# Performance work log

Hardware: AMD Instinct MI355X
Metric: run time of the kernel (lower is better)

The kernel has to match this reference:

```python
import jax, jax.numpy as jnp
import numpy as np

N = 100000       # nodes
E0 = 1600000     # random edges (self-loops appended -> E = E0 + N)
IN = 128         # input feature dim
H1, C1 = 8, 8    # conv1 heads, out channels per head
C2 = 64          # num_classes (conv2 out, heads=1)
NEG_SLOPE = 0.2


def gat_conv(x, src, dst, W, att_src, att_dst, bias, heads, out_ch, concat):
    """PyG-style GATConv (eval mode, no dropout). x: [N, F_in]."""
    n = x.shape[0]
    h = (x @ W).reshape(n, heads, out_ch)              # [N, H, C]
    a_src = jnp.sum(h * att_src, axis=-1)              # [N, H]
    a_dst = jnp.sum(h * att_dst, axis=-1)              # [N, H]
    e = jax.nn.leaky_relu(a_src[src] + a_dst[dst], NEG_SLOPE)  # [E, H]
    # segment softmax over edges grouped by destination node
    e_max = jax.ops.segment_max(e, dst, num_segments=n)
    ex = jnp.exp(e - e_max[dst])
    denom = jax.ops.segment_sum(ex, dst, num_segments=n)
    alpha = ex / denom[dst]                            # [E, H]
    msg = h[src] * alpha[:, :, None]                   # [E, H, C]
    out = jax.ops.segment_sum(msg, dst, num_segments=n)  # [N, H, C]
    out = out.reshape(n, heads * out_ch) if concat else out.mean(axis=1)
    return out + bias


def setup_inputs() -> dict:
    key = jax.random.key(0)
    ks = jax.random.split(key, 12)
    nodes = jnp.arange(N, dtype=jnp.int32)
    feat = jax.random.normal(ks[0], (N, IN), jnp.float32)
    src = jax.random.randint(ks[1], (E0,), 0, N, jnp.int32)
    dst = jax.random.randint(ks[2], (E0,), 0, N, jnp.int32)
    loop = jnp.arange(N, dtype=jnp.int32)
    edge_index = jnp.stack([jnp.concatenate([src, loop]),
                            jnp.concatenate([dst, loop])])  # [2, E]
    mask = jnp.ones((N,), bool)
    label = jax.random.randint(ks[3], (N,), 0, C2, jnp.int32)
    s = 0.1
    W1 = jax.random.normal(ks[4], (IN, H1 * C1), jnp.float32) * s
    att_src1 = jax.random.normal(ks[5], (H1, C1), jnp.float32) * s
    att_dst1 = jax.random.normal(ks[6], (H1, C1), jnp.float32) * s
    b1 = jnp.zeros((H1 * C1,), jnp.float32)
    W2 = jax.random.normal(ks[7], (H1 * C1, C2), jnp.float32) * s
    att_src2 = jax.random.normal(ks[8], (1, C2), jnp.float32) * s
    att_dst2 = jax.random.normal(ks[9], (1, C2), jnp.float32) * s
    b2 = jnp.zeros((C2,), jnp.float32)
    return {"nodes": nodes, "feat": feat, "edge_index": edge_index, "mask": mask,
            "label": label, "W1": W1, "att_src1": att_src1, "att_dst1": att_dst1,
            "b1": b1, "W2": W2, "att_src2": att_src2, "att_dst2": att_dst2, "b2": b2}


def reference(nodes, feat, edge_index, mask, label,
              W1, att_src1, att_dst1, b1, W2, att_src2, att_dst2, b2):
    src, dst = edge_index[0], edge_index[1]
    x = jax.nn.elu(gat_conv(feat, src, dst, W1, att_src1, att_dst1, b1,
                            H1, C1, concat=True))          # [N, 64]
    scores = gat_conv(x, src, dst, W2, att_src2, att_dst2, b2,
                      1, C2, concat=False)                  # [N, C2]
    logp = jax.nn.log_softmax(scores, axis=-1)
    nll = -jnp.take_along_axis(logp, label[:, None].astype(jnp.int32), axis=1)[:, 0]
    m = mask.astype(scores.dtype)
    loss = jnp.sum(nll * m) / jnp.sum(m)                    # masked mean CE
    pred = jnp.argmax(scores, axis=1)
    return loss, pred, label
```

## Files before the change

kernel.cpp:

```cpp
#include <hip/hip_runtime.h>
#include <cstdint>

#define NHEAD 8
#define D1 64
#define IN_F 128
#define NEG 0.2f
#define NBINS 256
#define BINS 1024
#define BSH 7
#define CHUNK 8192

__device__ __forceinline__ void fma4(float4& a, float s, const float4& v)
{
    a.x = fmaf(s, v.x, a.x); a.y = fmaf(s, v.y, a.y);
    a.z = fmaf(s, v.z, a.z); a.w = fmaf(s, v.w, a.w);
}

__global__ __launch_bounds__(256) void k_gemm1_hist(
    const float* __restrict__ feat,
    const float* __restrict__ W1,
    const float* __restrict__ att_s,
    const float* __restrict__ att_d,
    float* __restrict__ h1, float* __restrict__ a_src, float* __restrict__ a_dst,
    const int* __restrict__ dst, int* __restrict__ btot, int* __restrict__ bh,
    int N, int E, int GH)
{
    __shared__ float Wh[32 * 64];
    __shared__ float Fh[64 * 36];
    const int tid = threadIdx.x;

    if ((int)blockIdx.x < GH) {
        int* hist = (int*)Wh;
        for (int b = tid; b < BINS; b += 256) hist[b] = 0;
        __syncthreads();
        const int e0 = blockIdx.x * CHUNK;
        #pragma unroll
        for (int r = 0; r < 8; ++r) {
            int e = e0 + r * 1024 + tid * 4;
            if (e + 3 < E) {
                int4 d4 = *(const int4*)&dst[e];
                atomicAdd(&hist[d4.x >> BSH], 1);
                atomicAdd(&hist[d4.y >> BSH], 1);
                atomicAdd(&hist[d4.z >> BSH], 1);
                atomicAdd(&hist[d4.w >> BSH], 1);
            } else {
                for (int k = e; k < E && k < e + 4; ++k)
                    atomicAdd(&hist[dst[k] >> BSH], 1);
            }
        }
        __syncthreads();
        for (int b = tid; b < BINS; b += 256) {
            int c = hist[b];
            bh[(size_t)blockIdx.x * BINS + b] = c;
            if (c) atomicAdd(&btot[b * 16], c);
        }
        return;
    }

    const int tx = tid & 15, ty = tid >> 4;
    const int base = (blockIdx.x - GH) * 64;
    float4 acc0 = {0,0,0,0}, acc1 = {0,0,0,0}, acc2 = {0,0,0,0}, acc3 = {0,0,0,0};

    for (int p = 0; p < 4; ++p) {
        if (p) __syncthreads();
        for (int i = tid; i < 32 * 64; i += 256)
            Wh[i] = W1[p * 2048 + i];
        for (int i = tid; i < 64 * 32; i += 256) {
            int r = i >> 5, kk = i & 31;
            int n = base + r;
            Fh[r * 36 + kk] = (n < N) ? feat[(size_t)n * IN_F + p * 32 + kk] : 0.f;
        }
        __syncthreads();
        const float* wk = &Wh[4 * tx];
        const float* f0 = &Fh[(4 * ty + 0) * 36];
        const float* f1 = &Fh[(4 * ty + 1) * 36];
        const float* f2 = &Fh[(4 * ty + 2) * 36];
        const float* f3 = &Fh[(4 * ty + 3) * 36];
        #pragma unroll
        for (int kk = 0; kk < 32; kk += 4) {
            float4 fa = *(const float4*)&f0[kk];
            float4 fb = *(const float4*)&f1[kk];
            float4 fc = *(const float4*)&f2[kk];
            float4 fd = *(const float4*)&f3[kk];
            float4 w0 = *(const float4*)&wk[(kk + 0) * 64];
            float4 w1 = *(const float4*)&wk[(kk + 1) * 64];
            float4 w2 = *(const float4*)&wk[(kk + 2) * 64];
            float4 w3 = *(const float4*)&wk[(kk + 3) * 64];
            fma4(acc0, fa.x, w0); fma4(acc0, fa.y, w1); fma4(acc0, fa.z, w2); fma4(acc0, fa.w, w3);
            fma4(acc1, fb.x, w0); fma4(acc1, fb.y, w1); fma4(acc1, fb.z, w2); fma4(acc1, fb.w, w3);
            fma4(acc2, fc.x, w0); fma4(acc2, fc.y, w1); fma4(acc2, fc.z, w2); fma4(acc2, fc.w, w3);
            fma4(acc3, fd.x, w0); fma4(acc3, fd.y, w1); fma4(acc3, fd.z, w2); fma4(acc3, fd.w, w3);
        }
    }
    const float4 as4 = *(const float4*)&att_s[4 * tx];
    const float4 ad4 = *(const float4*)&att_d[4 * tx];
    float4 accs[4] = {acc0, acc1, acc2, acc3};
    #pragma unroll
    for (int i = 0; i < 4; ++i) {
        int n = base + 4 * ty + i;
        if (n < N) {
            *(float4*)&h1[(size_t)n * D1 + 4 * tx] = accs[i];
            float ps = accs[i].x * as4.x + accs[i].y * as4.y + accs[i].z * as4.z + accs[i].w * as4.w;
            float pd = accs[i].x * ad4.x + accs[i].y * ad4.y + accs[i].z * ad4.z + accs[i].w * ad4.w;
            ps += __shfl_xor(ps, 1);
            pd += __shfl_xor(pd, 1);
            if ((tx & 1) == 0) {
                a_src[n * NHEAD + (tx >> 1)] = ps;
                a_dst[n * NHEAD + (tx >> 1)] = pd;
            }
        }
    }
}

__device__ __forceinline__ int block_incl_scan(int v, int tid, int* lds4)
{
    int lane = tid & 63, w = tid >> 6;
    #pragma unroll
    for (int off = 1; off < 64; off <<= 1) {
        int t = __shfl_up(v, off);
        if (lane >= off) v += t;
    }
    if (lane == 63) lds4[w] = v;
    __syncthreads();
    int add = 0;
    #pragma unroll
    for (int i = 0; i < 4; ++i)
        if (i < w) add += lds4[i];
    __syncthreads();
    return v + add;
}

__global__ __launch_bounds__(256) void k_bscan(
    const int* __restrict__ btot, int* __restrict__ bbase, int* __restrict__ gcur,
    double* __restrict__ bins)
{
    __shared__ int lds4[4];
    const int tid = threadIdx.x;
    bins[tid] = 0.0;
    int c0 = btot[(4 * tid + 0) * 16];
    int c1 = btot[(4 * tid + 1) * 16];
    int c2 = btot[(4 * tid + 2) * 16];
    int c3 = btot[(4 * tid + 3) * 16];
    int v = c0 + c1 + c2 + c3;
    int incl = block_incl_scan(v, tid, lds4);
    int b0 = incl - v, b1 = b0 + c0, b2 = b1 + c1, b3 = b2 + c2;
    bbase[4 * tid + 0] = b0; gcur[(4 * tid + 0) * 16] = b0;
    bbase[4 * tid + 1] = b1; gcur[(4 * tid + 1) * 16] = b1;
    bbase[4 * tid + 2] = b2; gcur[(4 * tid + 2) * 16] = b2;
    bbase[4 * tid + 3] = b3; gcur[(4 * tid + 3) * 16] = b3;
}

__global__ __launch_bounds__(256) void k_scatter(
    const int* __restrict__ src, const int* __restrict__ dst,
    const int* __restrict__ bh, int* __restrict__ gcur,
    int* __restrict__ bucketed, int E)
{
    __shared__ int base[BINS], cur[BINS];
    const int tid = threadIdx.x;
    for (int b = tid; b < BINS; b += 256) {
        cur[b] = 0;
        int c = bh[(size_t)blockIdx.x * BINS + b];
        if (c) base[b] = atomicAdd(&gcur[b * 16], c);
    }
    __syncthreads();
    const int e0 = blockIdx.x * CHUNK;
    #pragma unroll
    for (int r = 0; r < 8; ++r) {
        int e = e0 + r * 1024 + tid * 4;
        if (e + 3 < E) {
            int4 d4 = *(const int4*)&dst[e];
            int4 s4 = *(const int4*)&src[e];
            int bx, rx;
            bx = d4.x >> BSH; rx = atomicAdd(&cur[bx], 1); bucketed[base[bx] + rx] = ((d4.x & 127) << 17) | s4.x;
            bx = d4.y >> BSH; rx = atomicAdd(&cur[bx], 1); bucketed[base[bx] + rx] = ((d4.y & 127) << 17) | s4.y;
            bx = d4.z >> BSH; rx = atomicAdd(&cur[bx], 1); bucketed[base[bx] + rx] = ((d4.z & 127) << 17) | s4.z;
            bx = d4.w >> BSH; rx = atomicAdd(&cur[bx], 1); bucketed[base[bx] + rx] = ((d4.w & 127) << 17) | s4.w;
        } else {
            for (int k = e; k < E && k < e + 4; ++k) {
                int d = dst[k];
                int bx = d >> BSH;
                int rx = atomicAdd(&cur[bx], 1);
                bucketed[base[bx] + rx] = ((d & 127) << 17) | src[k];
            }
        }
    }
}

__global__ __launch_bounds__(256) void k_seg(
    const int* __restrict__ btot, const int* __restrict__ bbase,
    const int* __restrict__ bucketed,
    int* __restrict__ deg, int* __restrict__ rowstart, int* __restrict__ srcs, int N)
{
    __shared__ int cnt[128], cur[128], lb[128];
    const int tid = threadIdx.x;
    const int b = blockIdx.x;
    const int gs = bbase[b];
    const int sz = btot[b * 16];
    if (tid < 128) { cnt[tid] = 0; cur[tid] = 0; }
    __syncthreads();
    for (int i = tid; i < sz; i += 256)
        atomicAdd(&cnt[bucketed[gs + i] >> 17], 1);
    __syncthreads();
    if (tid < 128) lb[tid] = cnt[tid];
    __syncthreads();
    #pragma unroll
    for (int off = 1; off < 128; off <<= 1) {
        int t = 0;
        if (tid < 128 && tid >= off) t = lb[tid - off];
        __syncthreads();
        if (tid < 128 && tid >= off) lb[tid] += t;
        __syncthreads();
    }
    if (tid < 128) {
        int ex = lb[tid] - cnt[tid];
        lb[tid] = ex;
        int d = b * 128 + tid;
        if (d < N) { deg[d] = cnt[tid]; rowstart[d] = gs + ex; }
    }
    __syncthreads();
    for (int i = tid; i < sz; i += 256) {
        int v = bucketed[gs + i];
        int d7 = v >> 17;
        int r = atomicAdd(&cur[d7], 1);
        srcs[gs + lb[d7] + r] = v & 0x1FFFF;
    }
}

__global__ __launch_bounds__(256) void k_agg1(
    const int* __restrict__ deg, const int* __restrict__ rowstart,
    const int* __restrict__ srcs,
    const float* __restrict__ a_s, const float* __restrict__ a_d,
    const float* __restrict__ h1, const float* __restrict__ b1,
    float* __restrict__ x, int N)
{
    const int tid = threadIdx.x, w = tid >> 6, j = tid & 63;
    const int c = j & 7, hh = j >> 3;
    const int n = blockIdx.x * 4 + w;
    if (n >= N) return;
    const int rlen = deg[n];
    const int row = rowstart[n];
    const float ad = a_d[n * NHEAD + hh];
    float acc0 = 0.f, acc1 = 0.f, den = 0.f;
    int m = rlen < 8 ? rlen : 8;
    int myS   = (c < m) ? srcs[row + c] : 0;
    float av  = (c < m) ? a_s[myS * NHEAD + hh] : 0.f;
    for (int base = 0; base < rlen; base += 8) {
        int mn = rlen - base - 8; if (mn > 8) mn = 8;
        int   myS_n = (c < mn) ? srcs[row + base + 8 + c] : 0;
        float av_n  = (c < mn) ? a_s[myS_n * NHEAD + hh] : 0.f;
        float ex = 0.f;
        if (c < m) {
            float v = av + ad;
            v = v > 0.f ? v : NEG * v;
            ex = expf(v);
        }
        float ds = ex;
        ds += __shfl_xor(ds, 1);
        ds += __shfl_xor(ds, 2);
        ds += __shfl_xor(ds, 4);
        den += ds;
        if (m == 8) {
            int   s8[8]; float e8[8], l8[8];
            #pragma unroll
            for (int k = 0; k < 8; ++k) {
                s8[k] = __builtin_amdgcn_readlane(myS, k);
                e8[k] = __shfl(ex, (j & 0x38) | k);
            }
            #pragma unroll
            for (int k = 0; k < 8; ++k)
                l8[k] = h1[(size_t)s8[k] * D1 + j];
            #pragma unroll
            for (int k = 0; k < 8; ++k) {
                if (k & 1) acc1 = fmaf(e8[k], l8[k], acc1);
                else       acc0 = fmaf(e8[k], l8[k], acc0);
            }
        } else {
            for (int k = 0; k < m; ++k) {
                int s = __shfl(myS, k);
                float exk = __shfl(ex, (j & 0x38) | k);
                if (k & 1) acc1 = fmaf(exk, h1[(size_t)s * D1 + j], acc1);
                else       acc0 = fmaf(exk, h1[(size_t)s * D1 + j], acc0);
            }
        }
        myS = myS_n; av = av_n; m = mn > 0 ? mn : 0;
    }
    float o = (acc0 + acc1) / den + b1[j];
    x[(size_t)n * D1 + j] = o > 0.f ? o : expm1f(o);
}

__global__ __launch_bounds__(256) void k_gemm2(
    const float* __restrict__ x,
    const float* __restrict__ W2,
    const float* __restrict__ att_s,
    const float* __restrict__ att_d,
    float* __restrict__ h2, float* __restrict__ a_src, float* __restrict__ a_dst,
    int N)
{
    __shared__ float Wh[64 * 64];
    __shared__ float Fh[64 * 68];
    const int tid = threadIdx.x;
    const int tx = tid & 15, ty = tid >> 4;
    const int base = blockIdx.x * 64;
    for (int i = tid; i < 64 * 64; i += 256)
        Wh[i] = W2[i];
    for (int i = tid; i < 64 * 64; i += 256) {
        int r = i >> 6, kk = i & 63;
        int n = base + r;
        Fh[r * 68 + kk] = (n < N) ? x[(size_t)n * 64 + kk] : 0.f;
    }
    __syncthreads();
    float4 acc0 = {0,0,0,0}, acc1 = {0,0,0,0}, acc2 = {0,0,0,0}, acc3 = {0,0,0,0};
    const float* wk = &Wh[4 * tx];
    const float* f0 = &Fh[(4 * ty + 0) * 68];
    const float* f1 = &Fh[(4 * ty + 1) * 68];
    const float* f2 = &Fh[(4 * ty + 2) * 68];
    const float* f3 = &Fh[(4 * ty + 3) * 68];
    #pragma unroll 4
    for (int kk = 0; kk < 64; kk += 4) {
        float4 fa = *(const float4*)&f0[kk];
        float4 fb = *(const float4*)&f1[kk];
        float4 fc = *(const float4*)&f2[kk];
        float4 fd = *(const float4*)&f3[kk];
        float4 w0 = *(const float4*)&wk[(kk + 0) * 64];
        float4 w1 = *(const float4*)&wk[(kk + 1) * 64];
        float4 w2 = *(const float4*)&wk[(kk + 2) * 64];
        float4 w3 = *(const float4*)&wk[(kk + 3) * 64];
        fma4(acc0, fa.x, w0); fma4(acc0, fa.y, w1); fma4(acc0, fa.z, w2); fma4(acc0, fa.w, w3);
        fma4(acc1, fb.x, w0); fma4(acc1, fb.y, w1); fma4(acc1, fb.z, w2); fma4(acc1, fb.w, w3);
        fma4(acc2, fc.x, w0); fma4(acc2, fc.y, w1); fma4(acc2, fc.z, w2); fma4(acc2, fc.w, w3);
        fma4(acc3, fd.x, w0); fma4(acc3, fd.y, w1); fma4(acc3, fd.z, w2); fma4(acc3, fd.w, w3);
    }
    const float4 as4 = *(const float4*)&att_s[4 * tx];
    const float4 ad4 = *(const float4*)&att_d[4 * tx];
    float4 accs[4] = {acc0, acc1, acc2, acc3};
    #pragma unroll
    for (int i = 0; i < 4; ++i) {
        int n = base + 4 * ty + i;
        if (n < N) {
            *(float4*)&h2[(size_t)n * 64 + 4 * tx] = accs[i];
            float ps = accs[i].x * as4.x + accs[i].y * as4.y + accs[i].z * as4.z + accs[i].w * as4.w;
            float pd = accs[i].x * ad4.x + accs[i].y * ad4.y + accs[i].z * ad4.z + accs[i].w * ad4.w;
            ps += __shfl_xor(ps, 1); pd += __shfl_xor(pd, 1);
            ps += __shfl_xor(ps, 2); pd += __shfl_xor(pd, 2);
            ps += __shfl_xor(ps, 4); pd += __shfl_xor(pd, 4);
            ps += __shfl_xor(ps, 8); pd += __shfl_xor(pd, 8);
            if (tx == 0) { a_src[n] = ps; a_dst[n] = pd; }
        }
    }
}

__global__ __launch_bounds__(256) void k_agg2(
    const int* __restrict__ deg, const int* __restrict__ rowstart,
    const int* __restrict__ srcs,
    const float* __restrict__ a_s, const float* __restrict__ a_d,
    const float* __restrict__ h2, const float* __restrict__ b2,
    const int* __restrict__ label,
    float* __restrict__ dout, double* __restrict__ bins, int N)
{
    __shared__ float snll[4];
    const int tid = threadIdx.x, w = tid >> 6, j = tid & 63;
    const int t = j & 15, q = j >> 4;
    const int n = blockIdx.x * 4 + w;
    if (j == 0) snll[w] = 0.f;
    if (n < N) {
        const int rlen = deg[n];
        const int row = rowstart[n];
        const float ad = a_d[n];
        float4 acc = {0.f, 0.f, 0.f, 0.f};
        float den = 0.f;
        for (int base = 0; base < rlen; base += 64) {
            int m = rlen - base; if (m > 64) m = 64;
            int myS = 0; float ex = 0.f;
            if (j < m) {
                myS = srcs[row + base + j];
                float v = a_s[myS] + ad;
                v = v > 0.f ? v : NEG * v;
                ex = expf(v);
            }
            float ds = ex;
            #pragma unroll
            for (int off = 1; off < 64; off <<= 1) ds += __shfl_xor(ds, off);
            den += ds;
            int eb = 0;
            for (; eb + 16 <= m; eb += 16) {
                int s4[4]; float e4[4]; float4 l4[4];
                #pragma unroll
                for (int ii = 0; ii < 4; ++ii) {
                    int e = eb + 4 * ii + q;
                    s4[ii] = __shfl(myS, e);
                    e4[ii] = __shfl(ex, e);
                }
                #pragma unroll
                for (int ii = 0; ii < 4; ++ii)
                    l4[ii] = *(const float4*)&h2[(size_t)s4[ii] * 64 + 4 * t];
                #pragma unroll
                for (int ii = 0; ii < 4; ++ii)
                    fma4(acc, e4[ii], l4[ii]);
            }
            for (; eb + 4 <= m; eb += 4) {
                int e = eb + q;
                int sk = __shfl(myS, e);
                float ek = __shfl(ex, e);
                float4 lk = *(const float4*)&h2[(size_t)sk * 64 + 4 * t];
                fma4(acc, ek, lk);
            }
            for (int k = eb; k < m; ++k) {
                int sk = __shfl(myS, k);
                float ek = __shfl(ex, k);
                if (q == (k & 3)) {
                    float4 lk = *(const float4*)&h2[(size_t)sk * 64 + 4 * t];
                    fma4(acc, ek, lk);
                }
            }
        }
        acc.x += __shfl_xor(acc.x, 16); acc.y += __shfl_xor(acc.y, 16);
        acc.z += __shfl_xor(acc.z, 16); acc.w += __shfl_xor(acc.w, 16);
        acc.x += __shfl_xor(acc.x, 32); acc.y += __shfl_xor(acc.y, 32);
        acc.z += __shfl_xor(acc.z, 32); acc.w += __shfl_xor(acc.w, 32);
        float4 b = *(const float4*)&b2[4 * t];
        float4 sc;
        sc.x = acc.x / den + b.x; sc.y = acc.y / den + b.y;
        sc.z = acc.z / den + b.z; sc.w = acc.w / den + b.w;
        float mv = sc.x; int mi = 4 * t;
        if (sc.y > mv) { mv = sc.y; mi = 4 * t + 1; }
        if (sc.z > mv) { mv = sc.z; mi = 4 * t + 2; }
        if (sc.w > mv) { mv = sc.w; mi = 4 * t + 3; }
        #pragma unroll
        for (int off = 1; off < 16; off <<= 1) {
            float ov = __shfl_xor(mv, off);
            int oi = __shfl_xor(mi, off);
            if (ov > mv || (ov == mv && oi < mi)) { mv = ov; mi = oi; }
        }
        float se = expf(sc.x - mv) + expf(sc.y - mv) + expf(sc.z - mv) + expf(sc.w - mv);
        #pragma unroll
        for (int off = 1; off < 16; off <<= 1) se += __shfl_xor(se, off);
        int lab = label[n];
        int comp = lab & 3;
        float cl = comp == 0 ? sc.x : comp == 1 ? sc.y : comp == 2 ? sc.z : sc.w;
        float sl = __shfl(cl, (j & 0x30) | (lab >> 2));
        if (j == 0) {
            snll[w] = mv + logf(se) - sl;
            dout[1 + n] = (float)mi;
            dout[1 + (size_t)N + n] = (float)lab;
        }
    }
    __syncthreads();
    if (tid == 0) {
        double bsum4 = (double)snll[0] + (double)snll[1]
                     + (double)snll[2] + (double)snll[3];
        atomicAdd(&bins[blockIdx.x & (NBINS - 1)], bsum4);
    }
}

__global__ __launch_bounds__(256) void k_loss(
    const double* __restrict__ bins, float* __restrict__ dout, int N)
{
    __shared__ double sw[4];
    const int tid = threadIdx.x;
    double v = bins[tid];
    #pragma unroll
    for (int off = 1; off < 64; off <<= 1) v += __shfl_xor(v, off);
    if ((tid & 63) == 0) sw[tid >> 6] = v;
    __syncthreads();
    if (tid == 0)
        dout[0] = (float)((sw[0] + sw[1] + sw[2] + sw[3]) / (double)N);
}

extern "C" void kernel_launch(void* const* d_in, const int* in_sizes, int n_in,
                              void* d_out, int out_size, void* d_ws, size_t ws_size,
                              hipStream_t stream)
{
    const float* feat   = (const float*)d_in[1];
    const int*   edge   = (const int*)d_in[2];
    const int*   label  = (const int*)d_in[4];
    const float* W1     = (const float*)d_in[5];
    const float* att_s1 = (const float*)d_in[6];
    const float* att_d1 = (const float*)d_in[7];
    const float* b1     = (const float*)d_in[8];
    const float* W2     = (const float*)d_in[9];
    const float* att_s2 = (const float*)d_in[10];
    const float* att_d2 = (const float*)d_in[11];
    const float* b2     = (const float*)d_in[12];

    const int N = in_sizes[0];
    const int E = in_sizes[2] / 2;
    const int* src = edge;
    const int* dst = edge + E;

    float* bufA = (float*)d_ws;
    float* bufB = bufA + (size_t)N * 64;
    float* a_s1 = bufB + (size_t)N * 64;
    float* a_d1 = a_s1 + (size_t)N * 8;
    int*   deg  = (int*)(a_d1 + (size_t)N * 8);
    int*   rowstart = deg + N;
    int*   srcs = rowstart + N;
    double* bins = (double*)(((uintptr_t)(srcs + E) + 7) & ~(uintptr_t)7);

    int* bucketed = (int*)bufB;
    int* btot  = bucketed + E;
    int* gcur  = btot + BINS * 16;
    int* bbase = gcur + BINS * 16;
    int* bh    = bbase + BINS;

    float* a_s2 = a_s1;
    float* a_d2 = a_s1 + N;

    float* out = (float*)d_out;

    const int GH    = (E + CHUNK - 1) / CHUNK;
    const int G1    = (N + 63) / 64;
    const int NBUCK = (N + 127) / 128;

    hipMemsetAsync(btot, 0, (size_t)BINS * 16 * sizeof(int), stream);

    k_gemm1_hist<<<GH + G1, 256, 0, stream>>>(feat, W1, att_s1, att_d1,
                                              bufA, a_s1, a_d1,
                                              dst, btot, bh, N, E, GH);
    k_bscan  <<<1, 256, 0, stream>>>(btot, bbase, gcur, bins);
    k_scatter<<<GH, 256, 0, stream>>>(src, dst, bh, gcur, bucketed, E);
    k_seg    <<<NBUCK, 256, 0, stream>>>(btot, bbase, bucketed, deg, rowstart, srcs, N);

    k_agg1 <<<(N + 3) / 4, 256, 0, stream>>>(deg, rowstart, srcs, a_s1, a_d1,
                                             bufA, b1, bufB, N);
    k_gemm2<<<G1, 256, 0, stream>>>(bufB, W2, att_s2, att_d2, bufA, a_s2, a_d2, N);
    k_agg2 <<<(N + 3) / 4, 256, 0, stream>>>(deg, rowstart, srcs, a_s2, a_d2,
                                             bufA, b2, label, out, bins, N);
    k_loss <<<1, 256, 0, stream>>>(bins, out, N);
}
```

Measured before the change: 428.4 us.

## Remap GAT aggregation lanes: float4 gathers in agg1, 16 lanes per node in agg2

```diff
diff --git a/kernel.cpp b/kernel.cpp
--- a/kernel.cpp
+++ b/kernel.cpp
@@ -235,17 +235,19 @@
 {
     const int tid = threadIdx.x, w = tid >> 6, j = tid & 63;
     const int c = j & 7, hh = j >> 3;
+    const int t = j & 15, q = j >> 4;
     const int n = blockIdx.x * 4 + w;
     if (n >= N) return;
     const int rlen = deg[n];
     const int row = rowstart[n];
     const float ad = a_d[n * NHEAD + hh];
-    float acc0 = 0.f, acc1 = 0.f, den = 0.f;
+    float4 acc = {0.f, 0.f, 0.f, 0.f};
+    float den = 0.f;
     int m = rlen < 8 ? rlen : 8;
     int myS   = (c < m) ? srcs[row + c] : 0;
     float av  = (c < m) ? a_s[myS * NHEAD + hh] : 0.f;
     for (int base = 0; base < rlen; base += 8) {
-        int mn = rlen - base - 8; if (mn > 8) mn = 8;
+        int mn = rlen - base - 8; if (mn > 8) mn = 8; if (mn < 0) mn = 0;
         int   myS_n = (c < mn) ? srcs[row + base + 8 + c] : 0;
         float av_n  = (c < mn) ? a_s[myS_n * NHEAD + hh] : 0.f;
         float ex = 0.f;
@@ -259,33 +261,32 @@
         ds += __shfl_xor(ds, 2);
         ds += __shfl_xor(ds, 4);
         den += ds;
-        if (m == 8) {
-            int   s8[8]; float e8[8], l8[8];
-            #pragma unroll
-            for (int k = 0; k < 8; ++k) {
-                s8[k] = __builtin_amdgcn_readlane(myS, k);
-                e8[k] = __shfl(ex, (j & 0x38) | k);
-            }
-            #pragma unroll
-            for (int k = 0; k < 8; ++k)
-                l8[k] = h1[(size_t)s8[k] * D1 + j];
-            #pragma unroll
-            for (int k = 0; k < 8; ++k) {
-                if (k & 1) acc1 = fmaf(e8[k], l8[k], acc1);
-                else       acc0 = fmaf(e8[k], l8[k], acc0);
-            }
-        } else {
-            for (int k = 0; k < m; ++k) {
-                int s = __shfl(myS, k);
-                float exk = __shfl(ex, (j & 0x38) | k);
-                if (k & 1) acc1 = fmaf(exk, h1[(size_t)s * D1 + j], acc1);
-                else       acc0 = fmaf(exk, h1[(size_t)s * D1 + j], acc0);
-            }
-        }
-        myS = myS_n; av = av_n; m = mn > 0 ? mn : 0;
-    }
-    float o = (acc0 + acc1) / den + b1[j];
-    x[(size_t)n * D1 + j] = o > 0.f ? o : expm1f(o);
+        int   s0 = __shfl(myS, 2 * q);
+        int   s1 = __shfl(myS, 2 * q + 1);
+        float e0 = __shfl(ex, ((t >> 1) << 3) | (2 * q));
+        float e1 = __shfl(ex, ((t >> 1) << 3) | (2 * q + 1));
+        float4 l0 = *(const float4*)&h1[(size_t)s0 * D1 + 4 * t];
+        float4 l1 = *(const float4*)&h1[(size_t)s1 * D1 + 4 * t];
+        fma4(acc, e0, l0);
+        fma4(acc, e1, l1);
+        myS = myS_n; av = av_n; m = mn;
+    }
+    acc.x += __shfl_xor(acc.x, 16); acc.y += __shfl_xor(acc.y, 16);
+    acc.z += __shfl_xor(acc.z, 16); acc.w += __shfl_xor(acc.w, 16);
+    acc.x += __shfl_xor(acc.x, 32); acc.y += __shfl_xor(acc.y, 32);
+    acc.z += __shfl_xor(acc.z, 32); acc.w += __shfl_xor(acc.w, 32);
+    float dd = __shfl(den, (t >> 1) << 3);
+    if (q == 0) {
+        float4 b = *(const float4*)&b1[4 * t];
+        float4 o;
+        o.x = acc.x / dd + b.x; o.y = acc.y / dd + b.y;
+        o.z = acc.z / dd + b.z; o.w = acc.w / dd + b.w;
+        o.x = o.x > 0.f ? o.x : expm1f(o.x);
+        o.y = o.y > 0.f ? o.y : expm1f(o.y);
+        o.z = o.z > 0.f ? o.z : expm1f(o.z);
+        o.w = o.w > 0.f ? o.w : expm1f(o.w);
+        *(float4*)&x[(size_t)n * D1 + 4 * t] = o;
+    }
 }
 
 __global__ __launch_bounds__(256) void k_gemm2(
@@ -357,98 +358,82 @@
     const int* __restrict__ label,
     float* __restrict__ dout, double* __restrict__ bins, int N)
 {
-    __shared__ float snll[4];
+    __shared__ int2 sx[4][64];
+    __shared__ float snll[16];
     const int tid = threadIdx.x, w = tid >> 6, j = tid & 63;
-    const int t = j & 15, q = j >> 4;
-    const int n = blockIdx.x * 4 + w;
-    if (j == 0) snll[w] = 0.f;
-    if (n < N) {
-        const int rlen = deg[n];
-        const int row = rowstart[n];
-        const float ad = a_d[n];
-        float4 acc = {0.f, 0.f, 0.f, 0.f};
-        float den = 0.f;
-        for (int base = 0; base < rlen; base += 64) {
-            int m = rlen - base; if (m > 64) m = 64;
-            int myS = 0; float ex = 0.f;
-            if (j < m) {
-                myS = srcs[row + base + j];
-                float v = a_s[myS] + ad;
-                v = v > 0.f ? v : NEG * v;
-                ex = expf(v);
-            }
-            float ds = ex;
-            #pragma unroll
-            for (int off = 1; off < 64; off <<= 1) ds += __shfl_xor(ds, off);
-            den += ds;
-            int eb = 0;
-            for (; eb + 16 <= m; eb += 16) {
-                int s4[4]; float e4[4]; float4 l4[4];
-                #pragma unroll
-                for (int ii = 0; ii < 4; ++ii) {
-                    int e = eb + 4 * ii + q;
-                    s4[ii] = __shfl(myS, e);
-                    e4[ii] = __shfl(ex, e);
-                }
-                #pragma unroll
-                for (int ii = 0; ii < 4; ++ii)
-                    l4[ii] = *(const float4*)&h2[(size_t)s4[ii] * 64 + 4 * t];
-                #pragma unroll
-                for (int ii = 0; ii < 4; ++ii)
-                    fma4(acc, e4[ii], l4[ii]);
-            }
-            for (; eb + 4 <= m; eb += 4) {
-                int e = eb + q;
-                int sk = __shfl(myS, e);
-                float ek = __shfl(ex, e);
-                float4 lk = *(const float4*)&h2[(size_t)sk * 64 + 4 * t];
-                fma4(acc, ek, lk);
-            }
-            for (int k = eb; k < m; ++k) {
-                int sk = __shfl(myS, k);
-                float ek = __shfl(ex, k);
-                if (q == (k & 3)) {
-                    float4 lk = *(const float4*)&h2[(size_t)sk * 64 + 4 * t];
-                    fma4(acc, ek, lk);
-                }
-            }
-        }
-        acc.x += __shfl_xor(acc.x, 16); acc.y += __shfl_xor(acc.y, 16);
-        acc.z += __shfl_xor(acc.z, 16); acc.w += __shfl_xor(acc.w, 16);
-        acc.x += __shfl_xor(acc.x, 32); acc.y += __shfl_xor(acc.y, 32);
-        acc.z += __shfl_xor(acc.z, 32); acc.w += __shfl_xor(acc.w, 32);
-        float4 b = *(const float4*)&b2[4 * t];
-        float4 sc;
-        sc.x = acc.x / den + b.x; sc.y = acc.y / den + b.y;
-        sc.z = acc.z / den + b.z; sc.w = acc.w / den + b.w;
-        float mv = sc.x; int mi = 4 * t;
-        if (sc.y > mv) { mv = sc.y; mi = 4 * t + 1; }
-        if (sc.z > mv) { mv = sc.z; mi = 4 * t + 2; }
-        if (sc.w > mv) { mv = sc.w; mi = 4 * t + 3; }
+    const int t = j & 15, g16 = j & 0x30;
+    const int n = blockIdx.x * 16 + (tid >> 4);
+    if (tid < 16) snll[tid] = 0.f;
+    __syncthreads();
+    const bool valid = (n < N);
+    const int rlen = valid ? deg[n] : 0;
+    const int row  = valid ? rowstart[n] : 0;
+    const float ad = valid ? a_d[n] : 0.f;
+    float4 acc = {0.f, 0.f, 0.f, 0.f};
+    float den = 0.f;
+    for (int base = 0; base < rlen; base += 16) {
+        int m = rlen - base; if (m > 16) m = 16;
+        int myS = 0; float ex = 0.f;
+        if (t < m) {
+            myS = srcs[row + base + t];
+            float v = a_s[myS] + ad;
+            v = v > 0.f ? v : NEG * v;
+            ex = expf(v);
+        }
+        float ds = ex;
+        ds += __shfl_xor(ds, 1); ds += __shfl_xor(ds, 2);
+        ds += __shfl_xor(ds, 4); ds += __shfl_xor(ds, 8);
+        den += ds;
+        sx[w][j] = make_int2(myS, __float_as_int(ex));
+        asm volatile("s_waitcnt lgkmcnt(0)" ::: "memory");
+        for (int kb = 0; kb < m; kb += 4) {
+            int2 p0 = sx[w][g16 | (kb + 0)];
+            int2 p1 = sx[w][g16 | (kb + 1)];
+            int2 p2 = sx[w][g16 | (kb + 2)];
+            int2 p3 = sx[w][g16 | (kb + 3)];
+            float4 l0 = *(const float4*)&h2[(size_t)p0.x * 64 + 4 * t];
+            float4 l1 = *(const float4*)&h2[(size_t)p1.x * 64 + 4 * t];
+            float4 l2 = *(const float4*)&h2[(size_t)p2.x * 64 + 4 * t];
+            float4 l3 = *(const float4*)&h2[(size_t)p3.x * 64 + 4 * t];
+            fma4(acc, __int_as_float(p0.y), l0);
+            fma4(acc, __int_as_float(p1.y), l1);
+            fma4(acc, __int_as_float(p2.y), l2);
+            fma4(acc, __int_as_float(p3.y), l3);
+        }
+        asm volatile("s_waitcnt lgkmcnt(0)" ::: "memory");
+    }
+    float4 b = *(const float4*)&b2[4 * t];
+    float4 sc;
+    sc.x = acc.x / den + b.x; sc.y = acc.y / den + b.y;
+    sc.z = acc.z / den + b.z; sc.w = acc.w / den + b.w;
+    float mv = sc.x; int mi = 4 * t;
+    if (sc.y > mv) { mv = sc.y; mi = 4 * t + 1; }
+    if (sc.z > mv) { mv = sc.z; mi = 4 * t + 2; }
+    if (sc.w > mv) { mv = sc.w; mi = 4 * t + 3; }
+    #pragma unroll
+    for (int off = 1; off < 16; off <<= 1) {
+        float ov = __shfl_xor(mv, off);
+        int oi = __shfl_xor(mi, off);
+        if (ov > mv || (ov == mv && oi < mi)) { mv = ov; mi = oi; }
+    }
+    float se = expf(sc.x - mv) + expf(sc.y - mv) + expf(sc.z - mv) + expf(sc.w - mv);
+    #pragma unroll
+    for (int off = 1; off < 16; off <<= 1) se += __shfl_xor(se, off);
+    int lab = valid ? label[n] : 0;
+    int comp = lab & 3;
+    float cl = comp == 0 ? sc.x : comp == 1 ? sc.y : comp == 2 ? sc.z : sc.w;
+    float sl = __shfl(cl, g16 | (lab >> 2));
+    if (t == 0 && valid) {
+        snll[tid >> 4] = mv + logf(se) - sl;
+        dout[1 + n] = (float)mi;
+        dout[1 + (size_t)N + n] = (float)lab;
+    }
+    __syncthreads();
+    if (tid == 0) {
+        double bs = 0.0;
         #pragma unroll
-        for (int off = 1; off < 16; off <<= 1) {
-            float ov = __shfl_xor(mv, off);
-            int oi = __shfl_xor(mi, off);
-            if (ov > mv || (ov == mv && oi < mi)) { mv = ov; mi = oi; }
-        }
-        float se = expf(sc.x - mv) + expf(sc.y - mv) + expf(sc.z - mv) + expf(sc.w - mv);
-        #pragma unroll
-        for (int off = 1; off < 16; off <<= 1) se += __shfl_xor(se, off);
-        int lab = label[n];
-        int comp = lab & 3;
-        float cl = comp == 0 ? sc.x : comp == 1 ? sc.y : comp == 2 ? sc.z : sc.w;
-        float sl = __shfl(cl, (j & 0x30) | (lab >> 2));
-        if (j == 0) {
-            snll[w] = mv + logf(se) - sl;
-            dout[1 + n] = (float)mi;
-            dout[1 + (size_t)N + n] = (float)lab;
-        }
-    }
-    __syncthreads();
-    if (tid == 0) {
-        double bsum4 = (double)snll[0] + (double)snll[1]
-                     + (double)snll[2] + (double)snll[3];
-        atomicAdd(&bins[blockIdx.x & (NBINS - 1)], bsum4);
+        for (int i = 0; i < 16; ++i) bs += (double)snll[i];
+        atomicAdd(&bins[blockIdx.x & (NBINS - 1)], bs);
     }
 }
 
@@ -523,7 +508,7 @@
     k_agg1 <<<(N + 3) / 4, 256, 0, stream>>>(deg, rowstart, srcs, a_s1, a_d1,
                                              bufA, b1, bufB, N);
     k_gemm2<<<G1, 256, 0, stream>>>(bufB, W2, att_s2, att_d2, bufA, a_s2, a_d2, N);
-    k_agg2 <<<(N + 3) / 4, 256, 0, stream>>>(deg, rowstart, srcs, a_s2, a_d2,
-                                             bufA, b2, label, out, bins, N);
+    k_agg2 <<<(N + 15) / 16, 256, 0, stream>>>(deg, rowstart, srcs, a_s2, a_d2,
+                                               bufA, b2, label, out, bins, N);
     k_loss <<<1, 256, 0, stream>>>(bins, out, N);
 }
```

Measured after the change: 397.8 us. 7.2% less time.
